# Optimization experiments

Measured on AMD Instinct MI355X. Metric: run time of the kernel, lower is better.

## Reference

```python
import jax, jax.numpy as jnp
import numpy as np

# Geometry constants (from init_kwargs)
B, A, D = 16, 720, 1024          # batch, n_projections, n_detector_pixels
H, W = 512, 512                  # reconstruction volume
VOL_SPACING = 1.0                # pixel spacing (world units)
DET_SPACING = 1.0                # detector pixel spacing
ANG_RANGE = np.pi                # 180 deg parallel beam


def setup_inputs() -> dict:
    key = jax.random.key(0)
    sinogram = jax.random.normal(key, (B, A, D), dtype=jnp.float32)
    # Ramp (Ram-Lak) filter in FFT domain: |f| (real-valued), length D.
    freqs = np.fft.fftfreq(D)
    filt = jnp.asarray(2.0 * np.abs(freqs), dtype=jnp.float32)
    return {"sinogram": sinogram, "filt": filt}


def reference(sinogram, filt):
    # --- FFT ramp filtering along detector axis (norm='ortho') ---
    x = jnp.fft.fft(sinogram, axis=-1, norm="ortho")
    x = x * filt                                   # complex * real broadcast over [B,A,D]
    x = jnp.fft.ifft(x, axis=-1, norm="ortho").real.astype(jnp.float32)

    # --- Parallel-beam backprojection onto [H,W] grid ---
    angles = jnp.linspace(0.0, ANG_RANGE, A, endpoint=False, dtype=jnp.float32)
    cs, sn = jnp.cos(angles), jnp.sin(angles)      # [A]
    px = (jnp.arange(W, dtype=jnp.float32) - (W - 1) / 2.0) * VOL_SPACING  # [W]
    py = (jnp.arange(H, dtype=jnp.float32) - (H - 1) / 2.0) * VOL_SPACING  # [H]
    px = px[None, :]                               # [1,W]
    py = py[:, None]                               # [H,1]
    det_center = (D - 1) / 2.0

    sino_t = jnp.transpose(x, (1, 0, 2))           # [A,B,D]

    def step(acc, inp):
        c, s, proj = inp                           # proj: [B,D]
        # detector coordinate of each pixel's ray for this angle
        t = (px * c + py * s) / DET_SPACING + det_center   # [H,W]
        i0 = jnp.floor(t)
        w = t - i0                                 # linear-interp weight
        i0i = i0.astype(jnp.int32)
        i1i = i0i + 1
        valid = (i0i >= 0) & (i1i <= D - 1)
        i0c = jnp.clip(i0i, 0, D - 1)
        i1c = jnp.clip(i1i, 0, D - 1)
        v = proj[:, i0c] * (1.0 - w) + proj[:, i1c] * w    # [B,H,W]
        return acc + jnp.where(valid, v, 0.0), None

    img0 = jnp.zeros((B, H, W), dtype=jnp.float32)
    img, _ = jax.lax.scan(step, img0, (cs, sn, sino_t))
    # angular integration weight (d_theta = pi / A)
    return img * jnp.float32(ANG_RANGE / A)
```

## Files before the change

kernel.cpp:

```cpp
#include <hip/hip_runtime.h>
#include <hip/hip_fp16.h>
#include <math.h>

#define NB 16
#define NA 720
#define ND 1024
#define NH 512
#define NW 512

#define TW 64
#define TH 8
#define PXT 2
#define NBT 8
#define WINN 68
#define GROUP 16

typedef __fp16 h2vec __attribute__((ext_vector_type(2)));

__device__ __forceinline__ uint32_t pkrtz_u32(float a, float b) {
    union { h2vec h; uint32_t u; } v;
    v.h = __builtin_amdgcn_cvt_pkrtz(a, b);
    return v.u;
}
__device__ __forceinline__ __half2 u32_to_h2(uint32_t u) {
    union { uint32_t u; __half2 h; } v; v.u = u; return v.h;
}
__device__ __forceinline__ uint32_t h2_to_u32(__half2 h) {
    union { __half2 h; uint32_t u; } v; v.h = h; return v.u;
}

__global__ __launch_bounds__(768) void prep_kernel(float4* __restrict__ ptable) {
    const int a = threadIdx.x;
    const int pos = blockIdx.x;
    if (a >= NA) return;
    const float step = (float)(M_PI / (double)NA);
    float s, c;
    sincosf((float)a * step, &s, &c);
    const int bx = pos & 7, by = pos >> 3;
    const float x0 = (float)(bx * TW) - 255.5f;
    const float x1 = x0 + (float)(TW - 1);
    const float y0 = (float)(by * TH) - 255.5f;
    const float tmin = 511.5f + fminf(x0 * c, x1 * c) + y0 * s;
    const int base = (int)floorf(tmin) - 1;
    ptable[pos * NA + a] = make_float4(c, s, 511.5f - (float)base,
                                       __int_as_float(a * ND + base));
}

__global__ __launch_bounds__(256) void filter_kernel(const float* __restrict__ sino,
                                                     const float* __restrict__ filt,
                                                     uint32_t* __restrict__ packed) {
    __shared__ float2 bufA[ND];
    __shared__ float2 bufB[ND];
    __shared__ float2 tw[ND / 2];

    const int tid = threadIdx.x;
    const int a = blockIdx.x;
    const int p = blockIdx.y;
    const float* __restrict__ xa = sino + ((size_t)(2 * p) * NA + a) * ND;
    const float* __restrict__ xb = xa + (size_t)NA * ND;
    uint32_t* __restrict__ yo = packed + ((size_t)(2 * p) * NA + a) * ND;

    #pragma unroll
    for (int i = 0; i < ND; i += 256)
        bufA[i + tid] = make_float2(xa[i + tid], xb[i + tid]);
    #pragma unroll
    for (int i = 0; i < ND / 2; i += 256) {
        int m = i + tid;
        float ang = (float)(-2.0 * M_PI / (double)ND) * (float)m;
        float s, c;
        sincosf(ang, &s, &c);
        tw[m] = make_float2(c, s);
    }
    __syncthreads();

    float2* src = bufA;
    float2* dst = bufB;

    for (int Ns = 1; Ns < ND; Ns <<= 1) {
        #pragma unroll
        for (int q = 0; q < ND / 2; q += 256) {
            int j = q + tid;
            int m = j & (Ns - 1);
            float2 v0 = src[j];
            float2 v1 = src[j + ND / 2];
            float2 w = tw[m * (ND / 2 / Ns)];
            float tr = w.x * v1.x - w.y * v1.y;
            float ti = w.x * v1.y + w.y * v1.x;
            int d = ((j & ~(Ns - 1)) << 1) + m;
            dst[d]      = make_float2(v0.x + tr, v0.y + ti);
            dst[d + Ns] = make_float2(v0.x - tr, v0.y - ti);
        }
        __syncthreads();
        float2* tmp = src; src = dst; dst = tmp;
    }

    const float SCALE = 1.0f / (float)ND;
    #pragma unroll
    for (int i = 0; i < ND; i += 256) {
        float f = filt[i + tid] * SCALE;
        src[i + tid].x *= f;
        src[i + tid].y *= f;
    }
    __syncthreads();

    for (int Ns = 1; Ns < ND; Ns <<= 1) {
        #pragma unroll
        for (int q = 0; q < ND / 2; q += 256) {
            int j = q + tid;
            int m = j & (Ns - 1);
            float2 v0 = src[j];
            float2 v1 = src[j + ND / 2];
            float2 w = tw[m * (ND / 2 / Ns)];
            float tr = w.x * v1.x + w.y * v1.y;
            float ti = w.x * v1.y - w.y * v1.x;
            int d = ((j & ~(Ns - 1)) << 1) + m;
            dst[d]      = make_float2(v0.x + tr, v0.y + ti);
            dst[d + Ns] = make_float2(v0.x - tr, v0.y - ti);
        }
        __syncthreads();
        float2* tmp = src; src = dst; dst = tmp;
    }

    #pragma unroll
    for (int i = 0; i < ND; i += 256)
        yo[i + tid] = pkrtz_u32(src[i + tid].x, src[i + tid].y);
}

__global__ __launch_bounds__(256, 4) void backproj_kernel(const uint32_t* __restrict__ packed,
                                                          const float4* __restrict__ ptable,
                                                          float* __restrict__ img) {
    __shared__ __align__(16) uint4 win[2][4][WINN];

    const int tid = threadIdx.x;
    const int bx = blockIdx.x, by = blockIdx.y, bz = blockIdx.z;

    const float4* __restrict__ pt = ptable + (size_t)((by << 3) + bx) * NA;

    const bool stg = tid < 2 * WINN;
    const int sg   = (tid >= WINN) ? 1 : 0;
    const int si   = tid - sg * WINN;
    const uint32_t* __restrict__ sbA =
        packed + (size_t)(2 * (4 * bz + 2 * sg)) * NA * ND + si;
    const uint32_t* __restrict__ sbB = sbA + (size_t)2 * NA * ND;
    uint4* const wptr = &win[sg][0][si];

    const int lane = tid & 63;
    const int wid  = tid >> 6;
    const int tx   = (wid << 4) + (lane & 15);
    const int ty0  = lane >> 4;
    const float px  = (float)(bx * TW + tx)  - 255.5f;
    const float pyf = (float)(by * TH + ty0) - 255.5f;

    float accf[8][PXT];
    __half2 hacc01[PXT], hacc23[PXT], hacc45[PXT], hacc67[PXT];
    #pragma unroll
    for (int k = 0; k < PXT; k++) {
        #pragma unroll
        for (int b = 0; b < 8; b++) accf[b][k] = 0.0f;
        hacc01[k] = u32_to_h2(0u); hacc23[k] = u32_to_h2(0u);
        hacc45[k] = u32_to_h2(0u); hacc67[k] = u32_to_h2(0u);
    }

    auto stage_load = [&](float4 P, uint2& wA, uint2& wB) {
        const int off = __float_as_int(P.w);
        const uint32_t* pa = sbA + off;
        const uint32_t* pb = sbB + off;
        wA = make_uint2(pa[0], pa[1]);
        wB = make_uint2(pb[0], pb[1]);
    };
    auto stage_write = [&](int ph, uint2 wA, uint2 wB) {
        wptr[ph * WINN] = make_uint4(
            wA.x, h2_to_u32(__hsub2(u32_to_h2(wA.y), u32_to_h2(wA.x))),
            wB.x, h2_to_u32(__hsub2(u32_to_h2(wB.y), u32_to_h2(wB.x))));
    };
    auto compute = [&](float4 P, int ph) {
        const float sy = P.y;
        const float tb = fmaf(px, P.x, fmaf(pyf, sy, P.z));
        #pragma unroll
        for (int k = 0; k < PXT; k++) {
            float t  = fmaf((float)(4 * k), sy, tb);
            int   i0 = (int)t;
#if __has_builtin(__builtin_amdgcn_fractf)
            float w  = __builtin_amdgcn_fractf(t);
#else
            float w  = t - (float)i0;
#endif
            __half2 wh2 = u32_to_h2(pkrtz_u32(w, w));
            const uint4 qA = win[0][ph][i0];
            const uint4 qB = win[1][ph][i0];
            hacc01[k] = __hfma2(wh2, u32_to_h2(qA.y), __hadd2(hacc01[k], u32_to_h2(qA.x)));
            hacc23[k] = __hfma2(wh2, u32_to_h2(qA.w), __hadd2(hacc23[k], u32_to_h2(qA.z)));
            hacc45[k] = __hfma2(wh2, u32_to_h2(qB.y), __hadd2(hacc45[k], u32_to_h2(qB.x)));
            hacc67[k] = __hfma2(wh2, u32_to_h2(qB.w), __hadd2(hacc67[k], u32_to_h2(qB.z)));
        }
    };

    uint2 h2A = make_uint2(0, 0), h2B = make_uint2(0, 0);
    uint2 h3A = make_uint2(0, 0), h3B = make_uint2(0, 0);
    if (stg) {
        uint2 wA, wB;
        stage_load(pt[0], wA, wB);  stage_write(0, wA, wB);
        stage_load(pt[1], wA, wB);  stage_write(1, wA, wB);
        stage_load(pt[2], h2A, h2B);
        stage_load(pt[3], h3A, h3B);
    }
    __syncthreads();

    for (int g = 0; g < NA; g += GROUP) {
        #pragma unroll 1
        for (int it = 0; it < GROUP / 4; it++) {
            const int a = g + it * 4;
            const float4 P0 = pt[a],     P1 = pt[a + 1];
            const float4 P2 = pt[a + 2], P3 = pt[a + 3];
            const float4 P4 = pt[min(a + 4, NA - 1)], P5 = pt[min(a + 5, NA - 1)];
            const float4 P6 = pt[min(a + 6, NA - 1)], P7 = pt[min(a + 7, NA - 1)];

            uint2 l4A = make_uint2(0, 0), l4B = make_uint2(0, 0);
            uint2 l5A = make_uint2(0, 0), l5B = make_uint2(0, 0);
            if (stg) {
                stage_load(P4, l4A, l4B);
                stage_load(P5, l5A, l5B);
                stage_write(2, h2A, h2B);
                stage_write(3, h3A, h3B);
            }
            compute(P0, 0);
            compute(P1, 1);
            __syncthreads();

            uint2 l6A = make_uint2(0, 0), l6B = make_uint2(0, 0);
            uint2 l7A = make_uint2(0, 0), l7B = make_uint2(0, 0);
            if (stg) {
                stage_load(P6, l6A, l6B);
                stage_load(P7, l7A, l7B);
                stage_write(0, l4A, l4B);
                stage_write(1, l5A, l5B);
            }
            compute(P2, 2);
            compute(P3, 3);
            h2A = l6A; h2B = l6B; h3A = l7A; h3B = l7B;
            __syncthreads();
        }
        #pragma unroll
        for (int k = 0; k < PXT; k++) {
            float2 v01 = __half22float2(hacc01[k]);
            float2 v23 = __half22float2(hacc23[k]);
            float2 v45 = __half22float2(hacc45[k]);
            float2 v67 = __half22float2(hacc67[k]);
            accf[0][k] += v01.x; accf[1][k] += v01.y;
            accf[2][k] += v23.x; accf[3][k] += v23.y;
            accf[4][k] += v45.x; accf[5][k] += v45.y;
            accf[6][k] += v67.x; accf[7][k] += v67.y;
            hacc01[k] = u32_to_h2(0u); hacc23[k] = u32_to_h2(0u);
            hacc45[k] = u32_to_h2(0u); hacc67[k] = u32_to_h2(0u);
        }
    }

    const float SCALE = (float)(M_PI / (double)NA);
    const size_t bstride = (size_t)NH * NW;
    size_t o0 = (((size_t)(bz * NBT) * NH) + (by * TH + ty0)) * NW + (bx * TW + tx);
    #pragma unroll
    for (int k = 0; k < PXT; k++) {
        #pragma unroll
        for (int b = 0; b < 8; b++)
            img[o0 + (size_t)(4 * k) * NW + (size_t)b * bstride] = accf[b][k] * SCALE;
    }
}

extern "C" void kernel_launch(void* const* d_in, const int* in_sizes, int n_in,
                              void* d_out, int out_size, void* d_ws, size_t ws_size,
                              hipStream_t stream) {
    const float* sino = (const float*)d_in[0];
    const float* filt = (const float*)d_in[1];
    float* out = (float*)d_out;

    const size_t pack_bytes = (size_t)NB * NA * ND * sizeof(uint32_t);
    const size_t ptab_bytes = (size_t)512 * NA * sizeof(float4);
    uint32_t* packed;
    float4* ptable;
    if (ws_size >= pack_bytes + ptab_bytes) {
        packed = (uint32_t*)d_ws;
        ptable = (float4*)((char*)d_ws + pack_bytes);
    } else {
        packed = (uint32_t*)d_in[0];
        ptable = (float4*)d_ws;
    }

    prep_kernel<<<dim3(512), dim3(768), 0, stream>>>(ptable);
    filter_kernel<<<dim3(NA, NB / 2), dim3(256), 0, stream>>>(sino, filt, packed);
    backproj_kernel<<<dim3(NW / TW, NH / TH, NB / NBT), dim3(256), 0, stream>>>(packed, ptable, out);
}
```

Before: 409.3 us.

## Use radix-4 Stockham FFT with swizzled LDS and remap backprojection pixel layout

The filter kernel's radix-2 Stockham FFT, which ran ten stages, becomes a radix-4 FFT with five stages, each thread doing one butterfly per stage. This halves the number of barriers and the LDS round trips. All shared-memory indices go through an XOR swizzle to cut bank conflicts, and the twiddle table grows to 768 entries. Separately, the backprojection thread-to-pixel mapping changes from a 16x4 lane layout with a vertical second pixel to an 8x8 layout with a horizontal second pixel offset by 8. That changes the detector-window access spread per wavefront and the store pattern.

```diff
diff --git a/kernel.cpp b/kernel.cpp
--- a/kernel.cpp
+++ b/kernel.cpp
@@ -46,12 +46,21 @@
                                        __int_as_float(a * ND + base));
 }
 
+#define SZ(i) ((i) ^ (((i) >> 4) & 15))
+
+__device__ __forceinline__ float2 cmul(float2 w, float2 v) {
+    return make_float2(w.x * v.x - w.y * v.y, w.x * v.y + w.y * v.x);
+}
+__device__ __forceinline__ float2 cmulc(float2 w, float2 v) {
+    return make_float2(w.x * v.x + w.y * v.y, w.x * v.y - w.y * v.x);
+}
+
 __global__ __launch_bounds__(256) void filter_kernel(const float* __restrict__ sino,
                                                      const float* __restrict__ filt,
                                                      uint32_t* __restrict__ packed) {
     __shared__ float2 bufA[ND];
     __shared__ float2 bufB[ND];
-    __shared__ float2 tw[ND / 2];
+    __shared__ float2 tw4[768];
 
     const int tid = threadIdx.x;
     const int a = blockIdx.x;
@@ -62,34 +71,41 @@
 
     #pragma unroll
     for (int i = 0; i < ND; i += 256)
-        bufA[i + tid] = make_float2(xa[i + tid], xb[i + tid]);
-    #pragma unroll
-    for (int i = 0; i < ND / 2; i += 256) {
+        bufA[SZ(i + tid)] = make_float2(xa[i + tid], xb[i + tid]);
+    #pragma unroll
+    for (int i = 0; i < 768; i += 256) {
         int m = i + tid;
         float ang = (float)(-2.0 * M_PI / (double)ND) * (float)m;
         float s, c;
         sincosf(ang, &s, &c);
-        tw[m] = make_float2(c, s);
+        tw4[SZ(m)] = make_float2(c, s);
     }
     __syncthreads();
 
     float2* src = bufA;
     float2* dst = bufB;
 
-    for (int Ns = 1; Ns < ND; Ns <<= 1) {
-        #pragma unroll
-        for (int q = 0; q < ND / 2; q += 256) {
-            int j = q + tid;
-            int m = j & (Ns - 1);
-            float2 v0 = src[j];
-            float2 v1 = src[j + ND / 2];
-            float2 w = tw[m * (ND / 2 / Ns)];
-            float tr = w.x * v1.x - w.y * v1.y;
-            float ti = w.x * v1.y + w.y * v1.x;
-            int d = ((j & ~(Ns - 1)) << 1) + m;
-            dst[d]      = make_float2(v0.x + tr, v0.y + ti);
-            dst[d + Ns] = make_float2(v0.x - tr, v0.y - ti);
-        }
+    for (int Ns = 1; Ns < ND; Ns <<= 2) {
+        const int j = tid;
+        const int m = j & (Ns - 1);
+        const int tstep = (ND / 4) / Ns;
+        float2 u0 = src[SZ(j)];
+        float2 x1 = src[SZ(j + 256)];
+        float2 x2 = src[SZ(j + 512)];
+        float2 x3 = src[SZ(j + 768)];
+        float2 w1 = tw4[SZ(m * tstep)];
+        float2 w2 = tw4[SZ(2 * m * tstep)];
+        float2 w3 = tw4[SZ(3 * m * tstep)];
+        float2 u1 = cmul(w1, x1), u2 = cmul(w2, x2), u3 = cmul(w3, x3);
+        float2 A  = make_float2(u0.x + u2.x, u0.y + u2.y);
+        float2 Bb = make_float2(u0.x - u2.x, u0.y - u2.y);
+        float2 C  = make_float2(u1.x + u3.x, u1.y + u3.y);
+        float2 D  = make_float2(u1.x - u3.x, u1.y - u3.y);
+        const int d = ((j & ~(Ns - 1)) << 2) + m;
+        dst[SZ(d)]          = make_float2(A.x + C.x, A.y + C.y);
+        dst[SZ(d + Ns)]     = make_float2(Bb.x + D.y, Bb.y - D.x);
+        dst[SZ(d + 2 * Ns)] = make_float2(A.x - C.x, A.y - C.y);
+        dst[SZ(d + 3 * Ns)] = make_float2(Bb.x - D.y, Bb.y + D.x);
         __syncthreads();
         float2* tmp = src; src = dst; dst = tmp;
     }
@@ -98,32 +114,41 @@
     #pragma unroll
     for (int i = 0; i < ND; i += 256) {
         float f = filt[i + tid] * SCALE;
-        src[i + tid].x *= f;
-        src[i + tid].y *= f;
+        src[SZ(i + tid)].x *= f;
+        src[SZ(i + tid)].y *= f;
     }
     __syncthreads();
 
-    for (int Ns = 1; Ns < ND; Ns <<= 1) {
-        #pragma unroll
-        for (int q = 0; q < ND / 2; q += 256) {
-            int j = q + tid;
-            int m = j & (Ns - 1);
-            float2 v0 = src[j];
-            float2 v1 = src[j + ND / 2];
-            float2 w = tw[m * (ND / 2 / Ns)];
-            float tr = w.x * v1.x + w.y * v1.y;
-            float ti = w.x * v1.y - w.y * v1.x;
-            int d = ((j & ~(Ns - 1)) << 1) + m;
-            dst[d]      = make_float2(v0.x + tr, v0.y + ti);
-            dst[d + Ns] = make_float2(v0.x - tr, v0.y - ti);
-        }
+    for (int Ns = 1; Ns < ND; Ns <<= 2) {
+        const int j = tid;
+        const int m = j & (Ns - 1);
+        const int tstep = (ND / 4) / Ns;
+        float2 u0 = src[SZ(j)];
+        float2 x1 = src[SZ(j + 256)];
+        float2 x2 = src[SZ(j + 512)];
+        float2 x3 = src[SZ(j + 768)];
+        float2 w1 = tw4[SZ(m * tstep)];
+        float2 w2 = tw4[SZ(2 * m * tstep)];
+        float2 w3 = tw4[SZ(3 * m * tstep)];
+        float2 u1 = cmulc(w1, x1), u2 = cmulc(w2, x2), u3 = cmulc(w3, x3);
+        float2 A  = make_float2(u0.x + u2.x, u0.y + u2.y);
+        float2 Bb = make_float2(u0.x - u2.x, u0.y - u2.y);
+        float2 C  = make_float2(u1.x + u3.x, u1.y + u3.y);
+        float2 D  = make_float2(u1.x - u3.x, u1.y - u3.y);
+        const int d = ((j & ~(Ns - 1)) << 2) + m;
+        dst[SZ(d)]          = make_float2(A.x + C.x, A.y + C.y);
+        dst[SZ(d + Ns)]     = make_float2(Bb.x - D.y, Bb.y + D.x);
+        dst[SZ(d + 2 * Ns)] = make_float2(A.x - C.x, A.y - C.y);
+        dst[SZ(d + 3 * Ns)] = make_float2(Bb.x + D.y, Bb.y - D.x);
         __syncthreads();
         float2* tmp = src; src = dst; dst = tmp;
     }
 
     #pragma unroll
-    for (int i = 0; i < ND; i += 256)
-        yo[i + tid] = pkrtz_u32(src[i + tid].x, src[i + tid].y);
+    for (int i = 0; i < ND; i += 256) {
+        float2 v = src[SZ(i + tid)];
+        yo[i + tid] = pkrtz_u32(v.x, v.y);
+    }
 }
 
 __global__ __launch_bounds__(256, 4) void backproj_kernel(const uint32_t* __restrict__ packed,
@@ -146,10 +171,10 @@
 
     const int lane = tid & 63;
     const int wid  = tid >> 6;
-    const int tx   = (wid << 4) + (lane & 15);
-    const int ty0  = lane >> 4;
-    const float px  = (float)(bx * TW + tx)  - 255.5f;
-    const float pyf = (float)(by * TH + ty0) - 255.5f;
+    const int tx0  = (wid << 4) + (lane & 7);
+    const int ty   = lane >> 3;
+    const float px  = (float)(bx * TW + tx0) - 255.5f;
+    const float pyf = (float)(by * TH + ty)  - 255.5f;
 
     float accf[8][PXT];
     __half2 hacc01[PXT], hacc23[PXT], hacc45[PXT], hacc67[PXT];
@@ -174,11 +199,10 @@
             wB.x, h2_to_u32(__hsub2(u32_to_h2(wB.y), u32_to_h2(wB.x))));
     };
     auto compute = [&](float4 P, int ph) {
-        const float sy = P.y;
-        const float tb = fmaf(px, P.x, fmaf(pyf, sy, P.z));
+        const float tb = fmaf(px, P.x, fmaf(pyf, P.y, P.z));
         #pragma unroll
         for (int k = 0; k < PXT; k++) {
-            float t  = fmaf((float)(4 * k), sy, tb);
+            float t  = fmaf((float)(8 * k), P.x, tb);
             int   i0 = (int)t;
 #if __has_builtin(__builtin_amdgcn_fractf)
             float w  = __builtin_amdgcn_fractf(t);
@@ -257,12 +281,12 @@
 
     const float SCALE = (float)(M_PI / (double)NA);
     const size_t bstride = (size_t)NH * NW;
-    size_t o0 = (((size_t)(bz * NBT) * NH) + (by * TH + ty0)) * NW + (bx * TW + tx);
+    size_t o0 = (((size_t)(bz * NBT) * NH) + (by * TH + ty)) * NW + (bx * TW + tx0);
     #pragma unroll
     for (int k = 0; k < PXT; k++) {
         #pragma unroll
         for (int b = 0; b < 8; b++)
-            img[o0 + (size_t)(4 * k) * NW + (size_t)b * bstride] = accf[b][k] * SCALE;
+            img[o0 + (size_t)(8 * k) + (size_t)b * bstride] = accf[b][k] * SCALE;
     }
 }
 
```

Result: faster. 377.1 us (-7.9%).
